# Kernel optimization log

Hardware: AMD Instinct MI355X
Metric: run time of the kernel (lower is better)

The kernel has to match this reference:

```python
import jax, jax.numpy as jnp
import numpy as np

B, NL, L1, D = 16, 12, 197, 768   # batch, num_layers, 1+num_patches, embed_dim
E, K, C, IMG = 4, 3, 21, 224      # num_experts, topk, num_classes, image_size


def setup_inputs() -> dict:
    key = jax.random.key(0)
    k0, k1, k2 = jax.random.split(key, 3)
    features = jax.random.normal(k0, (B, NL, L1, D), jnp.float32)
    gate_W = jax.random.normal(k1, (D, E), jnp.float32) / np.sqrt(D).astype(np.float32)
    gate_b = jnp.zeros((E,), jnp.float32)
    expert_W = jax.random.normal(k2, (E, D, C), jnp.float32) / np.sqrt(D).astype(np.float32)
    expert_b = jnp.zeros((E, C), jnp.float32)
    return dict(features=features, gate_W=gate_W, gate_b=gate_b,
                expert_W=expert_W, expert_b=expert_b)


def reference(features, gate_W, gate_b, expert_W, expert_b):
    cls_tokens = features[:, :, 0, :]          # [B, NL, D]
    feats = features[:, :, 1:, :]              # [B, NL, L, D]
    gate_score = cls_tokens @ gate_W + gate_b  # [B, NL, E]
    gate_prob = jax.nn.softmax(gate_score.transpose(0, 2, 1), axis=-1)  # [B, E, NL]
    # per-expert topk over layers (vectorized over experts)
    topv, topi = jax.lax.top_k(gate_prob, K)   # [B, E, K]
    # gather selected layer feature maps: [B, E, K, L, D]
    gathered = jnp.take_along_axis(feats[:, None], topi[:, :, :, None, None], axis=2)
    w = jax.nn.softmax(topv, axis=-1)          # re-softmax of topk values, [B, E, K]
    mixed = jnp.einsum('bek,bekld->beld', w, gathered)  # [B, E, L, D]
    # expert heads (UPerNet modeled as linear decode + bilinear upsample)
    logits = jnp.einsum('beld,edc->belc', mixed, expert_W) + expert_b[None, :, None, :]
    L = logits.shape[2]
    g = int(np.sqrt(L))                        # 14x14 patch grid
    logits = logits.reshape(B, E, g, g, C).transpose(0, 1, 4, 2, 3)  # [B,E,C,g,g]
    logits = jax.image.resize(logits, (B, E, C, IMG, IMG), method='bilinear')
    return logits.mean(axis=1)                 # mean over experts -> [B, C, IMG, IMG]
```

## Files before the change

### kernel.cpp

```cpp
#include <hip/hip_runtime.h>
#include <math.h>

#define B_ 16
#define NL_ 12
#define L1_ 197
#define D_ 768
#define E_ 4
#define K_ 3
#define C_ 21
#define IMG_ 224
#define LP_ 196
#define NJ_ 84
#define MT_ 52
#define KSTEPS 24

typedef __attribute__((ext_vector_type(8))) short short8;
typedef __attribute__((ext_vector_type(4))) float f32x4;
typedef unsigned short ushort_t;

__device__ __forceinline__ ushort_t bf16rne(float x) {
    unsigned u = __float_as_uint(x);
    unsigned r = (u + 0x7FFFu + ((u >> 16) & 1u)) >> 16;
    return (ushort_t)r;
}

__device__ __forceinline__ void select_be(const float* __restrict__ gs, int b, int e,
                                          int idx[3], float w[3]) {
    float p[NL_]; float mx = -1e30f;
    #pragma unroll
    for (int nl = 0; nl < NL_; ++nl) { float v = gs[(b * NL_ + nl) * E_ + e]; p[nl] = v; mx = fmaxf(mx, v); }
    float ss = 0.f;
    #pragma unroll
    for (int nl = 0; nl < NL_; ++nl) { p[nl] = expf(p[nl] - mx); ss += p[nl]; }
    float inv = 1.0f / ss;
    #pragma unroll
    for (int nl = 0; nl < NL_; ++nl) p[nl] *= inv;
    unsigned used = 0; float v[3];
    #pragma unroll
    for (int k = 0; k < 3; ++k) {
        float best = -1.f; int bi = 0;
        #pragma unroll
        for (int nl = 0; nl < NL_; ++nl)
            if (!((used >> nl) & 1u) && p[nl] > best) { best = p[nl]; bi = nl; }
        used |= 1u << bi; idx[k] = bi; v[k] = best;
    }
    float x1 = expf(v[1] - v[0]), x2 = expf(v[2] - v[0]);
    float isw = 1.0f / (1.0f + x1 + x2);
    w[0] = isw; w[1] = x1 * isw; w[2] = x2 * isw;
}

__global__ __launch_bounds__(256) void prep_kernel(
        const float* __restrict__ feat, const float* __restrict__ gW,
        const float* __restrict__ gb, const float* __restrict__ eW,
        ushort_t* __restrict__ WtB, float* __restrict__ gs) {
    int blk = blockIdx.x, t = threadIdx.x;
    if (blk < B_ * NL_) {
        if (t < 64) {
            const float* cls = feat + (size_t)blk * L1_ * D_;
            float a0 = 0.f, a1 = 0.f, a2 = 0.f, a3 = 0.f;
            for (int q = 0; q < D_ / 64; ++q) {
                int d = t + 64 * q;
                float x = cls[d];
                float4 w = *(const float4*)(gW + (size_t)d * E_);
                a0 += x * w.x; a1 += x * w.y; a2 += x * w.z; a3 += x * w.w;
            }
            for (int off = 32; off > 0; off >>= 1) {
                a0 += __shfl_down(a0, off); a1 += __shfl_down(a1, off);
                a2 += __shfl_down(a2, off); a3 += __shfl_down(a3, off);
            }
            if (t == 0) {
                gs[blk * E_ + 0] = a0 + gb[0]; gs[blk * E_ + 1] = a1 + gb[1];
                gs[blk * E_ + 2] = a2 + gb[2]; gs[blk * E_ + 3] = a3 + gb[3];
            }
        }
    } else {
        int j = blk - B_ * NL_;
        if (j < NJ_) {
            int e = j / C_, c = j % C_;
            for (int k = t; k < D_; k += 256)
                WtB[(size_t)j * D_ + k] = bf16rne(eW[((size_t)e * D_ + k) * C_ + c]);
        } else {
            for (int k = t; k < D_; k += 256) WtB[(size_t)j * D_ + k] = 0;
        }
    }
}

__global__ __launch_bounds__(256) void select_kernel(
        const float* __restrict__ gs, int* __restrict__ topi,
        float* __restrict__ wgt, int* __restrict__ list, int* __restrict__ nsel) {
    __shared__ int sidx[B_ * E_ * 3];
    __shared__ int wcnt[3];
    int t = threadIdx.x;
    if (t < B_ * E_) {
        int b = t >> 2, e = t & 3;
        int idx[3]; float w[3];
        select_be(gs, b, e, idx, w);
        #pragma unroll
        for (int k = 0; k < 3; ++k) {
            topi[t * 3 + k] = idx[k]; wgt[t * 3 + k] = w[k]; sidx[t * 3 + k] = idx[k];
        }
    }
    __syncthreads();
    int f = 0, rank = 0;
    if (t < B_ * NL_) {
        int b = t / NL_, nl = t % NL_;
        #pragma unroll
        for (int ek = 0; ek < 12; ++ek) f |= (sidx[b * 12 + ek] == nl);
        unsigned long long m = __ballot(f != 0);
        int lane = t & 63;
        rank = __popcll(m & ((1ull << lane) - 1ull));
        if (lane == 0) wcnt[t >> 6] = __popcll(m);
    }
    __syncthreads();
    if (t < B_ * NL_ && f) {
        int wv = t >> 6;
        int base = 0;
        if (wv > 0) base += wcnt[0];
        if (wv > 1) base += wcnt[1];
        list[base + rank] = t;
    }
    if (t == 0) nsel[0] = wcnt[0] + wcnt[1] + wcnt[2];
}

#define GLOAD(ks, A0, A1, W0v, W1v) do {                                        \
    int _k0 = (ks) * 32;                                                        \
    if (avalid) { const f32x4* _p = (const f32x4*)(arow_base + _k0);            \
                  A0 = _p[kg * 2]; A1 = _p[kg * 2 + 1]; }                       \
    W0v = *(const short8*)(brow0 + _k0 + kg * 8);                               \
    if (bvalid1) W1v = *(const short8*)(brow1 + _k0 + kg * 8);                  \
} while (0)

#define SSTORE(buf, A0, A1, W0v, W1v) do {                                      \
    short8 _av;                                                                 \
    _Pragma("unroll")                                                           \
    for (int _i = 0; _i < 4; ++_i) {                                            \
        _av[_i]     = (short)bf16rne(A0[_i]);                                   \
        _av[_i + 4] = (short)bf16rne(A1[_i]);                                   \
    }                                                                           \
    Ab[buf][r * 5 + aslotw] = _av;                                              \
    Bb[buf][r * 5 + aslotw] = W0v;                                              \
    if (bvalid1) Bb[buf][(64 + r) * 5 + aslotw] = W1v;                          \
} while (0)

#define COMPUTE(buf) do {                                                       \
    short8 _af = Ab[buf][aidx];                                                 \
    _Pragma("unroll")                                                           \
    for (int _nt = 0; _nt < 6; ++_nt)                                           \
        acc[_nt] = __builtin_amdgcn_mfma_f32_16x16x32_bf16(                     \
            _af, Bb[buf][bidx[_nt]], acc[_nt], 0, 0, 0);                        \
} while (0)

__global__ __launch_bounds__(256, 3) void gemm_kernel(
        const float* __restrict__ feat, const ushort_t* __restrict__ WtB,
        const int* __restrict__ list, const int* __restrict__ nsel,
        float* __restrict__ proj) {
    int blk = blockIdx.x;
    if (blk >= nsel[0] * 4) return;
    int tile = blk & 3;
    int bn = list[blk >> 2];
    int rows_real = min(MT_, LP_ - tile * MT_);

    __shared__ short8 Ab[4][64 * 5];
    __shared__ short8 Bb[4][96 * 5];

    int t = threadIdx.x;
    int w = t >> 6, lane = t & 63;
    int r = t >> 2, kg = t & 3;
    int aslotw = kg ^ (r & 3);
    bool avalid = r < rows_real;
    bool bvalid1 = t < 128;

    const float* arow_base = feat + ((size_t)bn * L1_ + 1 + tile * MT_ + r) * D_;
    const ushort_t* brow0 = WtB + (size_t)r * D_;
    const ushort_t* brow1 = WtB + (size_t)(64 + r) * D_;

    int arow = w * 16 + (lane & 15);
    int aidx = arow * 5 + ((lane >> 4) ^ (arow & 3));
    int bidx[6];
    #pragma unroll
    for (int nt = 0; nt < 6; ++nt) {
        int jr = nt * 16 + (lane & 15);
        bidx[nt] = jr * 5 + ((lane >> 4) ^ (jr & 3));
    }

    {
        f32x4 xa0 = {0,0,0,0}, xa1 = {0,0,0,0}, ya0 = {0,0,0,0}, ya1 = {0,0,0,0};
        short8 xb0 = (short8)0, xb1 = (short8)0, yb0 = (short8)0, yb1 = (short8)0;
        GLOAD(0, xa0, xa1, xb0, xb1);
        GLOAD(1, ya0, ya1, yb0, yb1);
        SSTORE(0, xa0, xa1, xb0, xb1);
        SSTORE(1, ya0, ya1, yb0, yb1);
    }
    __syncthreads();

    f32x4 acc[6];
    #pragma unroll
    for (int nt = 0; nt < 6; ++nt) acc[nt] = (f32x4)0.0f;

    for (int i = 0; i < KSTEPS / 2; ++i) {
        int s = 2 * i;
        int cur = (i & 1) * 2;
        f32x4 xa0 = {0,0,0,0}, xa1 = {0,0,0,0}, ya0 = {0,0,0,0}, ya1 = {0,0,0,0};
        short8 xb0, xb1, yb0, yb1;
        if (s + 2 < KSTEPS) {
            GLOAD(s + 2, xa0, xa1, xb0, xb1);
            GLOAD(s + 3, ya0, ya1, yb0, yb1);
        }
        COMPUTE(cur);
        COMPUTE(cur + 1);
        if (s + 2 < KSTEPS) {
            SSTORE(cur ^ 2, xa0, xa1, xb0, xb1);
            SSTORE((cur ^ 2) + 1, ya0, ya1, yb0, yb1);
        }
        __syncthreads();
    }

    int lr = w * 16 + ((lane >> 4) << 2);
    int l0 = tile * MT_ + lr;
    if (lr < MT_ && l0 < LP_) {
        #pragma unroll
        for (int nt = 0; nt < 6; ++nt) {
            int j = nt * 16 + (lane & 15);
            if (j < NJ_)
                *(f32x4*)(proj + ((size_t)bn * NJ_ + j) * LP_ + l0) = acc[nt];
        }
    }
}

__global__ __launch_bounds__(256) void upsample_kernel(
        const float* __restrict__ proj, const int* __restrict__ topi,
        const float* __restrict__ wgt, const float* __restrict__ eb,
        float* __restrict__ out) {
    int bq = blockIdx.x;
    int q = bq & 7;
    int bc = bq >> 3;
    int b = bc / C_, c = bc % C_;
    int t = threadIdx.x;
    __shared__ float s[LP_];
    if (t < LP_) {
        float a = 0.25f * (eb[c] + eb[C_ + c] + eb[2 * C_ + c] + eb[3 * C_ + c]);
        #pragma unroll
        for (int e = 0; e < E_; ++e) {
            int base = (b * E_ + e) * 3;
            #pragma unroll
            for (int k = 0; k < 3; ++k) {
                int nl = topi[base + k];
                float wv = 0.25f * wgt[base + k];
                a += wv * proj[(((size_t)b * NL_ + nl) * NJ_ + e * C_ + c) * LP_ + t];
            }
        }
        s[t] = a;
    }
    __syncthreads();
    f32x4* out4 = (f32x4*)out + (size_t)bc * IMG_ * (IMG_ / 4);
    for (int i = t; i < 28 * 56; i += 256) {
        int oy = q * 28 + i / 56;
        int ox4 = (i % 56) * 4;
        float fy = (oy + 0.5f) * 0.0625f - 0.5f;
        fy = fminf(fmaxf(fy, 0.0f), 13.0f);
        int y0 = (int)fy;
        float ty = fy - (float)y0;
        int y1 = min(y0 + 1, 13);
        const float* r0 = s + y0 * 14;
        const float* r1 = s + y1 * 14;
        f32x4 res;
        #pragma unroll
        for (int u = 0; u < 4; ++u) {
            int ox = ox4 + u;
            float fx = (ox + 0.5f) * 0.0625f - 0.5f;
            fx = fminf(fmaxf(fx, 0.0f), 13.0f);
            int x0 = (int)fx;
            float tx = fx - (float)x0;
            int x1 = min(x0 + 1, 13);
            float v00 = r0[x0], v01 = r0[x1];
            float v10 = r1[x0], v11 = r1[x1];
            float top = v00 + tx * (v01 - v00);
            float bot = v10 + tx * (v11 - v10);
            res[u] = top + ty * (bot - top);
        }
        __builtin_nontemporal_store(res, &out4[oy * 56 + (i % 56)]);
    }
}

extern "C" void kernel_launch(void* const* d_in, const int* in_sizes, int n_in,
                              void* d_out, int out_size, void* d_ws, size_t ws_size,
                              hipStream_t stream) {
    const float* feat = (const float*)d_in[0];
    const float* gW   = (const float*)d_in[1];
    const float* gb   = (const float*)d_in[2];
    const float* eW   = (const float*)d_in[3];
    const float* eb   = (const float*)d_in[4];
    float* out = (float*)d_out;

    float* ws = (float*)d_ws;
    float*    gs   = ws;
    int*      topi = (int*)(ws + 768);
    float*    wgt  = ws + 960;
    int*      list = (int*)(ws + 1152);
    int*      nsel = (int*)(ws + 1344);
    ushort_t* WtB  = (ushort_t*)(ws + 1536);
    float*    proj = ws + 38400;

    hipLaunchKernelGGL(prep_kernel, dim3(B_ * NL_ + 96), dim3(256), 0, stream,
                       feat, gW, gb, eW, WtB, gs);
    hipLaunchKernelGGL(select_kernel, dim3(1), dim3(256), 0, stream,
                       gs, topi, wgt, list, nsel);
    hipLaunchKernelGGL(gemm_kernel, dim3(B_ * NL_ * 4), dim3(256), 0, stream,
                       feat, WtB, list, nsel, proj);
    hipLaunchKernelGGL(upsample_kernel, dim3(B_ * C_ * 8), dim3(256), 0, stream,
                       proj, topi, wgt, eb, out);
}
```

Before: 52.08 us.

## Load GEMM tiles directly global-to-LDS and convert A to bf16 after LDS read

New measurement: 51.40 us (median of 2 runs). No clear change (-1.3%).

```diff
diff --git a/kernel.cpp b/kernel.cpp
--- a/kernel.cpp
+++ b/kernel.cpp
@@ -22,6 +22,12 @@
     unsigned u = __float_as_uint(x);
     unsigned r = (u + 0x7FFFu + ((u >> 16) & 1u)) >> 16;
     return (ushort_t)r;
+}
+
+__device__ __forceinline__ void glds16(const void* g, void* l) {
+    __builtin_amdgcn_global_load_lds(
+        (const __attribute__((address_space(1))) unsigned int*)g,
+        (__attribute__((address_space(3))) unsigned int*)l, 16, 0, 0);
 }
 
 __device__ __forceinline__ void select_be(const float* __restrict__ gs, int b, int e,
@@ -122,35 +128,7 @@
     if (t == 0) nsel[0] = wcnt[0] + wcnt[1] + wcnt[2];
 }
 
-#define GLOAD(ks, A0, A1, W0v, W1v) do {                                        \
-    int _k0 = (ks) * 32;                                                        \
-    if (avalid) { const f32x4* _p = (const f32x4*)(arow_base + _k0);            \
-                  A0 = _p[kg * 2]; A1 = _p[kg * 2 + 1]; }                       \
-    W0v = *(const short8*)(brow0 + _k0 + kg * 8);                               \
-    if (bvalid1) W1v = *(const short8*)(brow1 + _k0 + kg * 8);                  \
-} while (0)
-
-#define SSTORE(buf, A0, A1, W0v, W1v) do {                                      \
-    short8 _av;                                                                 \
-    _Pragma("unroll")                                                           \
-    for (int _i = 0; _i < 4; ++_i) {                                            \
-        _av[_i]     = (short)bf16rne(A0[_i]);                                   \
-        _av[_i + 4] = (short)bf16rne(A1[_i]);                                   \
-    }                                                                           \
-    Ab[buf][r * 5 + aslotw] = _av;                                              \
-    Bb[buf][r * 5 + aslotw] = W0v;                                              \
-    if (bvalid1) Bb[buf][(64 + r) * 5 + aslotw] = W1v;                          \
-} while (0)
-
-#define COMPUTE(buf) do {                                                       \
-    short8 _af = Ab[buf][aidx];                                                 \
-    _Pragma("unroll")                                                           \
-    for (int _nt = 0; _nt < 6; ++_nt)                                           \
-        acc[_nt] = __builtin_amdgcn_mfma_f32_16x16x32_bf16(                     \
-            _af, Bb[buf][bidx[_nt]], acc[_nt], 0, 0, 0);                        \
-} while (0)
-
-__global__ __launch_bounds__(256, 3) void gemm_kernel(
+__global__ __launch_bounds__(256, 4) void gemm_kernel(
         const float* __restrict__ feat, const ushort_t* __restrict__ WtB,
         const int* __restrict__ list, const int* __restrict__ nsel,
         float* __restrict__ proj) {
@@ -160,67 +138,82 @@
     int bn = list[blk >> 2];
     int rows_real = min(MT_, LP_ - tile * MT_);
 
-    __shared__ short8 Ab[4][64 * 5];
-    __shared__ short8 Bb[4][96 * 5];
+    __shared__ f32x4  As4[2][64 * 8];
+    __shared__ short8 Bs[2][96 * 4];
 
     int t = threadIdx.x;
     int w = t >> 6, lane = t & 63;
-    int r = t >> 2, kg = t & 3;
-    int aslotw = kg ^ (r & 3);
-    bool avalid = r < rows_real;
-    bool bvalid1 = t < 128;
-
-    const float* arow_base = feat + ((size_t)bn * L1_ + 1 + tile * MT_ + r) * D_;
-    const ushort_t* brow0 = WtB + (size_t)r * D_;
-    const ushort_t* brow1 = WtB + (size_t)(64 + r) * D_;
-
-    int arow = w * 16 + (lane & 15);
-    int aidx = arow * 5 + ((lane >> 4) ^ (arow & 3));
+    int la = lane & 15, kp = lane >> 4;
+
+    const float* fbase = feat + ((size_t)bn * L1_ + 1 + tile * MT_) * D_;
+    int sA0 = w * 128 + lane;
+    int sA1 = sA0 + 64;
+    int rA0 = sA0 >> 3, qA0 = (sA0 & 7) ^ (rA0 & 7);
+    int rA1 = sA1 >> 3, qA1 = (sA1 & 7) ^ (rA1 & 7);
+    const float* gA0 = fbase + (size_t)min(rA0, rows_real - 1) * D_ + qA0 * 4;
+    const float* gA1 = fbase + (size_t)min(rA1, rows_real - 1) * D_ + qA1 * 4;
+
+    int sB0 = w * 64 + lane;
+    int jB0 = sB0 >> 2, cB0 = sB0 & 3;
+    int kgB0 = cB0 ^ (jB0 & 3) ^ (((jB0 >> 2) & 1) << 1);
+    const ushort_t* gB0 = WtB + (size_t)jB0 * D_ + kgB0 * 8;
+    int sB1 = 256 + w * 64 + lane;
+    int jB1 = sB1 >> 2, cB1 = sB1 & 3;
+    int kgB1 = cB1 ^ (jB1 & 3) ^ (((jB1 >> 2) & 1) << 1);
+    const ushort_t* gB1 = WtB + (size_t)jB1 * D_ + kgB1 * 8;
+    bool doB1 = (w < 2);
+
+    int arow = w * 16 + la;
+    int ar0 = arow * 8 + ((kp * 2) ^ (arow & 7));
     int bidx[6];
     #pragma unroll
     for (int nt = 0; nt < 6; ++nt) {
-        int jr = nt * 16 + (lane & 15);
-        bidx[nt] = jr * 5 + ((lane >> 4) ^ (jr & 3));
-    }
-
-    {
-        f32x4 xa0 = {0,0,0,0}, xa1 = {0,0,0,0}, ya0 = {0,0,0,0}, ya1 = {0,0,0,0};
-        short8 xb0 = (short8)0, xb1 = (short8)0, yb0 = (short8)0, yb1 = (short8)0;
-        GLOAD(0, xa0, xa1, xb0, xb1);
-        GLOAD(1, ya0, ya1, yb0, yb1);
-        SSTORE(0, xa0, xa1, xb0, xb1);
-        SSTORE(1, ya0, ya1, yb0, yb1);
-    }
+        int j = nt * 16 + la;
+        bidx[nt] = j * 4 + (kp ^ (j & 3) ^ (((j >> 2) & 1) << 1));
+    }
+
+    glds16(gA0, &As4[0][w * 128]);
+    glds16(gA1, &As4[0][w * 128 + 64]);
+    glds16(gB0, &Bs[0][w * 64]);
+    if (doB1) glds16(gB1, &Bs[0][256 + w * 64]);
     __syncthreads();
 
     f32x4 acc[6];
     #pragma unroll
     for (int nt = 0; nt < 6; ++nt) acc[nt] = (f32x4)0.0f;
 
-    for (int i = 0; i < KSTEPS / 2; ++i) {
-        int s = 2 * i;
-        int cur = (i & 1) * 2;
-        f32x4 xa0 = {0,0,0,0}, xa1 = {0,0,0,0}, ya0 = {0,0,0,0}, ya1 = {0,0,0,0};
-        short8 xb0, xb1, yb0, yb1;
-        if (s + 2 < KSTEPS) {
-            GLOAD(s + 2, xa0, xa1, xb0, xb1);
-            GLOAD(s + 3, ya0, ya1, yb0, yb1);
-        }
-        COMPUTE(cur);
-        COMPUTE(cur + 1);
-        if (s + 2 < KSTEPS) {
-            SSTORE(cur ^ 2, xa0, xa1, xb0, xb1);
-            SSTORE((cur ^ 2) + 1, ya0, ya1, yb0, yb1);
+    for (int s = 0; s < KSTEPS; ++s) {
+        int cur = s & 1;
+        if (s + 1 < KSTEPS) {
+            int k0 = (s + 1) * 32;
+            glds16(gA0 + k0, &As4[cur ^ 1][w * 128]);
+            glds16(gA1 + k0, &As4[cur ^ 1][w * 128 + 64]);
+            glds16(gB0 + k0, &Bs[cur ^ 1][w * 64]);
+            if (doB1) glds16(gB1 + k0, &Bs[cur ^ 1][256 + w * 64]);
+        }
+        {
+            f32x4 a0 = As4[cur][ar0];
+            f32x4 a1 = As4[cur][ar0 ^ 1];
+            short8 af;
+            #pragma unroll
+            for (int i = 0; i < 4; ++i) {
+                af[i]     = (short)bf16rne(a0[i]);
+                af[i + 4] = (short)bf16rne(a1[i]);
+            }
+            #pragma unroll
+            for (int nt = 0; nt < 6; ++nt)
+                acc[nt] = __builtin_amdgcn_mfma_f32_16x16x32_bf16(
+                    af, Bs[cur][bidx[nt]], acc[nt], 0, 0, 0);
         }
         __syncthreads();
     }
 
-    int lr = w * 16 + ((lane >> 4) << 2);
+    int lr = w * 16 + (kp << 2);
     int l0 = tile * MT_ + lr;
     if (lr < MT_ && l0 < LP_) {
         #pragma unroll
         for (int nt = 0; nt < 6; ++nt) {
-            int j = nt * 16 + (lane & 15);
+            int j = nt * 16 + la;
             if (j < NJ_)
                 *(f32x4*)(proj + ((size_t)bn * NJ_ + j) * LP_ + l0) = acc[nt];
         }
```
